# Kernel tuning notes

Measured on AMD Instinct MI355X. Metric: run time of the kernel, lower is better.

Reference implementation:

```python
import jax, jax.numpy as jnp
import numpy as np

INPUT_DIM = 256
UNITS = 256
BATCH = 65536


def _glorot(key, shape):
    fan_in, fan_out = shape
    limit = np.sqrt(6.0 / (fan_in + fan_out)).astype(np.float32)
    return jax.random.uniform(key, shape, jnp.float32, -limit, limit)


def setup_inputs() -> dict:
    key = jax.random.key(0)
    ks = jax.random.split(key, 8)
    d = {
        "inputs": jax.random.normal(ks[0], (BATCH, INPUT_DIM), jnp.float32),
        "h_prev": jax.random.normal(ks[1], (BATCH, UNITS), jnp.float32),
        "c_prev": jax.random.normal(ks[2], (BATCH, UNITS), jnp.float32),
        "W_f": _glorot(ks[3], (INPUT_DIM + UNITS, UNITS)),
        "W_i": _glorot(ks[4], (INPUT_DIM + UNITS, UNITS)),
        "W_c": _glorot(ks[5], (INPUT_DIM + UNITS, UNITS)),
        "W_o": _glorot(ks[6], (INPUT_DIM + UNITS, UNITS)),
        "b_f": jnp.zeros((UNITS,), jnp.float32),
        "b_i": jnp.zeros((UNITS,), jnp.float32),
        "b_c": jnp.zeros((UNITS,), jnp.float32),
        "b_o": jnp.zeros((UNITS,), jnp.float32),
    }
    return d


def reference(inputs, h_prev, c_prev, W_f, W_i, W_c, W_o, b_f, b_i, b_c, b_o):
    # z: [B, input_dim + units]
    z = jnp.concatenate([inputs, h_prev], axis=-1)
    f = jax.nn.sigmoid(z @ W_f + b_f)
    i = jax.nn.sigmoid(z @ W_i + b_i)
    c_tilde = jnp.tanh(z @ W_c + b_c)
    c = f * c_prev + i * c_tilde
    o = jax.nn.sigmoid(z @ W_o + b_o)
    h = o * jnp.tanh(c)
    return h, c
```

## Files before the change

### kernel.cpp

```cpp
#include <hip/hip_runtime.h>
#include <hip/hip_bf16.h>
#include <stdint.h>

#define BATCH   65536
#define UNITS   256
#define NCHUNK  8
#define ROWP    72
#define GSZ     (64 * ROWP)
#define SMEM_BYTES 65536

using f32x16 = __attribute__((ext_vector_type(16))) float;
using bf16x8 = __attribute__((ext_vector_type(8))) short;

__device__ __forceinline__ short f2bf(float f) {
  union { float f; unsigned u; } v; v.f = f;
  unsigned r = v.u + 0x7FFFu + ((v.u >> 16) & 1u);
  return (short)(r >> 16);
}
__device__ __forceinline__ float bf2f(short s) {
  union { float f; unsigned u; } v; v.u = ((unsigned)(unsigned short)s) << 16;
  return v.f;
}
__device__ __forceinline__ unsigned pk2(float a, float b) {
  union { __hip_bfloat162 h; unsigned u; } cv;
  cv.h = __float22bfloat162_rn(make_float2(a, b));
  return cv.u;
}

#define BAR() do { asm volatile("s_waitcnt lgkmcnt(0)" ::: "memory"); \
                   __builtin_amdgcn_s_barrier(); } while (0)

__global__ void cvt_weights(const float* __restrict__ Wf, const float* __restrict__ Wi,
                            const float* __restrict__ Wc, const float* __restrict__ Wo,
                            short* __restrict__ Wt) {
  int idx = blockIdx.x * 256 + threadIdx.x;
  int g   = idx >> 17;
  int k   = (idx >> 8) & 511;
  int col = idx & 255;
  const float* W = (g == 0) ? Wf : (g == 1) ? Wi : (g == 2) ? Wc : Wo;
  float val = W[k * 256 + col];
  int nb = col >> 6, n = col & 63;
  int c = k >> 6, kg = (k >> 3) & 7, k8 = k & 7;
  int out = ((((g * 4 + nb) * 8 + c) * 8 + kg) * 64 + n) * 8 + k8;
  Wt[out] = f2bf(val);
}

__global__ __launch_bounds__(256, 2) void lstm_fused(
    const float* __restrict__ x, const float* __restrict__ hprev,
    const float* __restrict__ cprev, const short* __restrict__ Wt,
    const float* __restrict__ bfp, const float* __restrict__ bip,
    const float* __restrict__ bcp, const float* __restrict__ bop,
    float* __restrict__ hout, float* __restrict__ cout)
{
  extern __shared__ __align__(16) char smem[];
  const int tid  = threadIdx.x;
  const int g    = tid >> 6;
  const int lane = tid & 63;
  const int la   = lane & 31;
  const int hh   = lane >> 5;

  int bid = blockIdx.x;
  int wg  = (bid & 7) * 512 + (bid >> 3);
  const int m0 = (wg >> 2) * 64;
  const int nb = wg & 3;
  const int n0 = nb * 64;

  const short* Bbase = Wt + ((size_t)(g * 4 + nb)) * 32768 + hh * 512 + la * 8;

  f32x16 acc[2][2] = {};
  bf16x8 bregA[8], bregB[8];

  auto loadB = [&](int c, bf16x8* br) {
#pragma unroll
    for (int ks = 0; ks < 4; ++ks) {
      const short* Bc = Bbase + (size_t)c * 4096 + ks * 1024;
      br[2 * ks]     = *(const bf16x8*)(Bc);
      br[2 * ks + 1] = *(const bf16x8*)(Bc + 256);
    }
  };
  auto compute = [&](int c, const bf16x8* br) {
#pragma unroll
    for (int ks = 0; ks < 4; ++ks) {
      const int kg  = c * 8 + 2 * ks + hh;
      const int off = kg * 1024 + ((la * 16) ^ ((kg & 7) << 4));
      bf16x8 a0 = *(const bf16x8*)(smem + off);
      bf16x8 a1 = *(const bf16x8*)(smem + off + 512);
      acc[0][0] = __builtin_amdgcn_mfma_f32_32x32x16_bf16(a0, br[2*ks],   acc[0][0], 0, 0, 0);
      acc[0][1] = __builtin_amdgcn_mfma_f32_32x32x16_bf16(a0, br[2*ks+1], acc[0][1], 0, 0, 0);
      acc[1][0] = __builtin_amdgcn_mfma_f32_32x32x16_bf16(a1, br[2*ks],   acc[1][0], 0, 0, 0);
      acc[1][1] = __builtin_amdgcn_mfma_f32_32x32x16_bf16(a1, br[2*ks+1], acc[1][1], 0, 0, 0);
    }
  };

  loadB(0, bregA);
  {
    const float4* xt = (const float4*)(x     + (size_t)m0 * 256);
    const float4* ht = (const float4*)(hprev + (size_t)m0 * 256);
    float4 vx[16], vh[16];
#pragma unroll
    for (int i = 0; i < 16; ++i) vx[i] = xt[tid + 256 * i];
#pragma unroll
    for (int i = 0; i < 16; ++i) vh[i] = ht[tid + 256 * i];
#pragma unroll
    for (int i = 0; i < 16; ++i) {
      const int idx = tid + 256 * i;
      const int row = idx >> 6, k4 = idx & 63;
      const int kg = k4 >> 1, half = k4 & 1;
      const int sub = (row * 16 + half * 8) ^ ((kg & 7) << 4);
      uint2 ux; ux.x = pk2(vx[i].x, vx[i].y); ux.y = pk2(vx[i].z, vx[i].w);
      *(uint2*)(smem + kg * 1024 + sub) = ux;
      uint2 uh; uh.x = pk2(vh[i].x, vh[i].y); uh.y = pk2(vh[i].z, vh[i].w);
      *(uint2*)(smem + (kg + 32) * 1024 + sub) = uh;
    }
  }
  BAR();

#pragma unroll
  for (int c = 0; c < NCHUNK; ++c) {
    bf16x8* cur = (c & 1) ? bregB : bregA;
    bf16x8* nxt = (c & 1) ? bregA : bregB;
    if (c + 1 < NCHUNK) loadB(c + 1, nxt);
    __builtin_amdgcn_s_setprio(1);
    compute(c, cur);
    __builtin_amdgcn_s_setprio(0);
  }

  const int ccol = tid & 63;
  const int rg   = tid >> 6;
  const size_t gbase = (size_t)(m0 + rg * 16) * 256 + n0 + ccol;
  float cp[16];
#pragma unroll
  for (int j = 0; j < 16; ++j) cp[j] = cprev[gbase + (size_t)j * 256];
  BAR();

  const float* bptr = (g == 0) ? bfp : (g == 1) ? bip : (g == 2) ? bcp : bop;
  const float bias0 = bptr[n0 + la];
  const float bias1 = bptr[n0 + 32 + la];
  short* G = (short*)smem;
#pragma unroll
  for (int mi = 0; mi < 2; ++mi)
#pragma unroll
    for (int ni = 0; ni < 2; ++ni) {
      const float bias = ni ? bias1 : bias0;
      const int   col  = la + ni * 32;
#pragma unroll
      for (int rq = 0; rq < 4; ++rq) {
        const int row0 = rq * 8 + 4 * hh + mi * 32;
        float t[4];
#pragma unroll
        for (int e = 0; e < 4; ++e) {
          float vv = acc[mi][ni][rq * 4 + e] + bias;
          t[e] = (g == 2) ? (1.f - 2.f / (__expf(2.f * vv) + 1.f))
                          : (1.f / (1.f + __expf(-vv)));
        }
        uint2 u; u.x = pk2(t[0], t[1]); u.y = pk2(t[2], t[3]);
        *(uint2*)(G + g * GSZ + col * ROWP + row0) = u;
      }
    }
  BAR();

  {
    const short* Gp = G + ccol * ROWP + rg * 16;
    bf16x8 gf[4][2];
#pragma unroll
    for (int gg = 0; gg < 4; ++gg) {
      gf[gg][0] = *(const bf16x8*)(Gp + gg * GSZ);
      gf[gg][1] = *(const bf16x8*)(Gp + gg * GSZ + 8);
    }
#pragma unroll
    for (int j = 0; j < 16; ++j) {
      float fg = bf2f(gf[0][j >> 3][j & 7]);
      float ig = bf2f(gf[1][j >> 3][j & 7]);
      float cg = bf2f(gf[2][j >> 3][j & 7]);
      float og = bf2f(gf[3][j >> 3][j & 7]);
      float cnew = fg * cp[j] + ig * cg;
      float hnew = og * (1.f - 2.f / (__expf(2.f * cnew) + 1.f));
      hout[gbase + (size_t)j * 256] = hnew;
      cout[gbase + (size_t)j * 256] = cnew;
    }
  }
}

extern "C" void kernel_launch(void* const* d_in, const int* in_sizes, int n_in,
                              void* d_out, int out_size, void* d_ws, size_t ws_size,
                              hipStream_t stream) {
  const float* x     = (const float*)d_in[0];
  const float* hprev = (const float*)d_in[1];
  const float* cprev = (const float*)d_in[2];
  const float* Wf    = (const float*)d_in[3];
  const float* Wi    = (const float*)d_in[4];
  const float* Wc    = (const float*)d_in[5];
  const float* Wo    = (const float*)d_in[6];
  const float* bfp   = (const float*)d_in[7];
  const float* bip   = (const float*)d_in[8];
  const float* bcp   = (const float*)d_in[9];
  const float* bop   = (const float*)d_in[10];
  float* out = (float*)d_out;
  short* Wt  = (short*)d_ws;

  cvt_weights<<<2048, 256, 0, stream>>>(Wf, Wi, Wc, Wo, Wt);

  lstm_fused<<<dim3(4096), dim3(256), SMEM_BYTES, stream>>>(
      x, hprev, cprev, Wt, bfp, bip, bcp, bop,
      out, out + (size_t)BATCH * UNITS);
}
```

Before: 152.9 us.

## Split each gate's column tile across two waves with 4-deep weight prefetch

```diff
diff --git a/kernel.cpp b/kernel.cpp
--- a/kernel.cpp
+++ b/kernel.cpp
@@ -4,7 +4,7 @@
 
 #define BATCH   65536
 #define UNITS   256
-#define NCHUNK  8
+#define NCH     16
 #define ROWP    72
 #define GSZ     (64 * ROWP)
 #define SMEM_BYTES 65536
@@ -26,9 +26,17 @@
   cv.h = __float22bfloat162_rn(make_float2(a, b));
   return cv.u;
 }
+#define LOG2E 1.4426950408889634f
+__device__ __forceinline__ float fast_sigmoid(float x) {
+  return __builtin_amdgcn_rcpf(1.f + __builtin_amdgcn_exp2f(x * -LOG2E));
+}
+__device__ __forceinline__ float fast_tanh(float x) {
+  return 2.f * __builtin_amdgcn_rcpf(1.f + __builtin_amdgcn_exp2f(x * (-2.f * LOG2E))) - 1.f;
+}
 
 #define BAR() do { asm volatile("s_waitcnt lgkmcnt(0)" ::: "memory"); \
                    __builtin_amdgcn_s_barrier(); } while (0)
+#define WAITV(n) asm volatile("s_waitcnt vmcnt(" #n ")" ::: "memory")
 
 __global__ void cvt_weights(const float* __restrict__ Wf, const float* __restrict__ Wi,
                             const float* __restrict__ Wc, const float* __restrict__ Wo,
@@ -39,13 +47,13 @@
   int col = idx & 255;
   const float* W = (g == 0) ? Wf : (g == 1) ? Wi : (g == 2) ? Wc : Wo;
   float val = W[k * 256 + col];
-  int nb = col >> 6, n = col & 63;
-  int c = k >> 6, kg = (k >> 3) & 7, k8 = k & 7;
-  int out = ((((g * 4 + nb) * 8 + c) * 8 + kg) * 64 + n) * 8 + k8;
+  int nt = col >> 5;
+  int c = k >> 5, ks = (k >> 4) & 1, hi = (k >> 3) & 1, e = k & 7;
+  int out = ((((g * 8 + nt) * 16 + c) * 2 + ks) * 64 + hi * 32 + (col & 31)) * 8 + e;
   Wt[out] = f2bf(val);
 }
 
-__global__ __launch_bounds__(256, 2) void lstm_fused(
+__global__ __launch_bounds__(512, 4) void lstm_fused(
     const float* __restrict__ x, const float* __restrict__ hprev,
     const float* __restrict__ cprev, const short* __restrict__ Wt,
     const float* __restrict__ bfp, const float* __restrict__ bip,
@@ -54,7 +62,9 @@
 {
   extern __shared__ __align__(16) char smem[];
   const int tid  = threadIdx.x;
-  const int g    = tid >> 6;
+  const int w    = tid >> 6;
+  const int g    = w & 3;
+  const int nh   = w >> 2;
   const int lane = tid & 63;
   const int la   = lane & 31;
   const int hh   = lane >> 5;
@@ -62,121 +72,105 @@
   int bid = blockIdx.x;
   int wg  = (bid & 7) * 512 + (bid >> 3);
   const int m0 = (wg >> 2) * 64;
-  const int nb = wg & 3;
-  const int n0 = nb * 64;
-
-  const short* Bbase = Wt + ((size_t)(g * 4 + nb)) * 32768 + hh * 512 + la * 8;
-
-  f32x16 acc[2][2] = {};
-  bf16x8 bregA[8], bregB[8];
-
-  auto loadB = [&](int c, bf16x8* br) {
-#pragma unroll
-    for (int ks = 0; ks < 4; ++ks) {
-      const short* Bc = Bbase + (size_t)c * 4096 + ks * 1024;
-      br[2 * ks]     = *(const bf16x8*)(Bc);
-      br[2 * ks + 1] = *(const bf16x8*)(Bc + 256);
+  const int nt = wg & 3;
+  const int n0 = nt * 64;
+
+  const short* Bbase = Wt + (size_t)(g * 8 + nt * 2 + nh) * 16384;
+
+  f32x16 acc[2] = {};
+  bf16x8 bB[4][2];
+
+  auto loadB = [&](int c) {
+    const short* p = Bbase + c * 1024 + lane * 8;
+    bB[c & 3][0] = *(const bf16x8*)(p);
+    bB[c & 3][1] = *(const bf16x8*)(p + 512);
+  };
+
+#pragma unroll
+  for (int i = 0; i < 16; ++i) {
+    const int idx  = tid + 512 * i;
+    const int row  = idx >> 7;
+    const int k4   = idx & 127;
+    const float* src = (k4 < 64)
+        ? (x     + (size_t)(m0 + row) * 256 + k4 * 4)
+        : (hprev + (size_t)(m0 + row) * 256 + (k4 - 64) * 4);
+    float4 v = *(const float4*)src;
+    const int c   = k4 >> 3, ks = (k4 >> 2) & 1, hi2 = (k4 >> 1) & 1;
+    const int e4  = (k4 & 1) * 4;
+    const int mh  = row >> 5, r31 = row & 31;
+    const int swz = (((c << 1) | ks) & 7) << 4;
+    const int byte = ((c * 2 + mh) * 2 + ks) * 1024
+                   + ((hi2 * 512 + r31 * 16) ^ swz) + e4 * 2;
+    uint2 u; u.x = pk2(v.x, v.y); u.y = pk2(v.z, v.w);
+    *(uint2*)(smem + byte) = u;
+  }
+  loadB(0); loadB(1); loadB(2); loadB(3);
+  BAR();
+
+#pragma unroll
+  for (int c = 0; c < NCH; ++c) {
+    if      (c <  NCH - 3) { WAITV(6); }
+    else if (c == NCH - 3) { WAITV(4); }
+    else if (c == NCH - 2) { WAITV(2); }
+    else                   { WAITV(0); }
+#pragma unroll
+    for (int ks = 0; ks < 2; ++ks) {
+      const int swz = (((c << 1) | ks) & 7) << 4;
+      const int b0  = ((c * 2 + 0) * 2 + ks) * 1024 + ((lane * 16) ^ swz);
+      const int b1  = ((c * 2 + 1) * 2 + ks) * 1024 + ((lane * 16) ^ swz);
+      bf16x8 a0 = *(const bf16x8*)(smem + b0);
+      bf16x8 a1 = *(const bf16x8*)(smem + b1);
+      acc[0] = __builtin_amdgcn_mfma_f32_32x32x16_bf16(a0, bB[c & 3][ks], acc[0], 0, 0, 0);
+      acc[1] = __builtin_amdgcn_mfma_f32_32x32x16_bf16(a1, bB[c & 3][ks], acc[1], 0, 0, 0);
     }
-  };
-  auto compute = [&](int c, const bf16x8* br) {
-#pragma unroll
-    for (int ks = 0; ks < 4; ++ks) {
-      const int kg  = c * 8 + 2 * ks + hh;
-      const int off = kg * 1024 + ((la * 16) ^ ((kg & 7) << 4));
-      bf16x8 a0 = *(const bf16x8*)(smem + off);
-      bf16x8 a1 = *(const bf16x8*)(smem + off + 512);
-      acc[0][0] = __builtin_amdgcn_mfma_f32_32x32x16_bf16(a0, br[2*ks],   acc[0][0], 0, 0, 0);
-      acc[0][1] = __builtin_amdgcn_mfma_f32_32x32x16_bf16(a0, br[2*ks+1], acc[0][1], 0, 0, 0);
-      acc[1][0] = __builtin_amdgcn_mfma_f32_32x32x16_bf16(a1, br[2*ks],   acc[1][0], 0, 0, 0);
-      acc[1][1] = __builtin_amdgcn_mfma_f32_32x32x16_bf16(a1, br[2*ks+1], acc[1][1], 0, 0, 0);
+    if (c + 4 < NCH) loadB(c + 4);
+  }
+
+  const int ccol = tid & 63;
+  const int rs   = tid >> 6;
+  const size_t gb = (size_t)(m0 + rs * 8) * 256 + n0 + ccol;
+  BAR();
+
+  float cp[8];
+#pragma unroll
+  for (int j = 0; j < 8; ++j) cp[j] = cprev[gb + (size_t)j * 256];
+
+  const float* bptr = (g == 0) ? bfp : (g == 1) ? bip : (g == 2) ? bcp : bop;
+  const float bias = bptr[n0 + nh * 32 + la];
+  short* G = (short*)smem;
+#pragma unroll
+  for (int mi = 0; mi < 2; ++mi) {
+    const int col = nh * 32 + la;
+#pragma unroll
+    for (int rq = 0; rq < 4; ++rq) {
+      const int row0 = rq * 8 + 4 * hh + mi * 32;
+      float t[4];
+#pragma unroll
+      for (int e = 0; e < 4; ++e) {
+        float vv = acc[mi][rq * 4 + e] + bias;
+        t[e] = (g == 2) ? fast_tanh(vv) : fast_sigmoid(vv);
+      }
+      uint2 u; u.x = pk2(t[0], t[1]); u.y = pk2(t[2], t[3]);
+      *(uint2*)(G + (g * 64 + col) * ROWP + row0) = u;
     }
-  };
-
-  loadB(0, bregA);
+  }
+  BAR();
+
   {
-    const float4* xt = (const float4*)(x     + (size_t)m0 * 256);
-    const float4* ht = (const float4*)(hprev + (size_t)m0 * 256);
-    float4 vx[16], vh[16];
-#pragma unroll
-    for (int i = 0; i < 16; ++i) vx[i] = xt[tid + 256 * i];
-#pragma unroll
-    for (int i = 0; i < 16; ++i) vh[i] = ht[tid + 256 * i];
-#pragma unroll
-    for (int i = 0; i < 16; ++i) {
-      const int idx = tid + 256 * i;
-      const int row = idx >> 6, k4 = idx & 63;
-      const int kg = k4 >> 1, half = k4 & 1;
-      const int sub = (row * 16 + half * 8) ^ ((kg & 7) << 4);
-      uint2 ux; ux.x = pk2(vx[i].x, vx[i].y); ux.y = pk2(vx[i].z, vx[i].w);
-      *(uint2*)(smem + kg * 1024 + sub) = ux;
-      uint2 uh; uh.x = pk2(vh[i].x, vh[i].y); uh.y = pk2(vh[i].z, vh[i].w);
-      *(uint2*)(smem + (kg + 32) * 1024 + sub) = uh;
-    }
-  }
-  BAR();
-
-#pragma unroll
-  for (int c = 0; c < NCHUNK; ++c) {
-    bf16x8* cur = (c & 1) ? bregB : bregA;
-    bf16x8* nxt = (c & 1) ? bregA : bregB;
-    if (c + 1 < NCHUNK) loadB(c + 1, nxt);
-    __builtin_amdgcn_s_setprio(1);
-    compute(c, cur);
-    __builtin_amdgcn_s_setprio(0);
-  }
-
-  const int ccol = tid & 63;
-  const int rg   = tid >> 6;
-  const size_t gbase = (size_t)(m0 + rg * 16) * 256 + n0 + ccol;
-  float cp[16];
-#pragma unroll
-  for (int j = 0; j < 16; ++j) cp[j] = cprev[gbase + (size_t)j * 256];
-  BAR();
-
-  const float* bptr = (g == 0) ? bfp : (g == 1) ? bip : (g == 2) ? bcp : bop;
-  const float bias0 = bptr[n0 + la];
-  const float bias1 = bptr[n0 + 32 + la];
-  short* G = (short*)smem;
-#pragma unroll
-  for (int mi = 0; mi < 2; ++mi)
-#pragma unroll
-    for (int ni = 0; ni < 2; ++ni) {
-      const float bias = ni ? bias1 : bias0;
-      const int   col  = la + ni * 32;
-#pragma unroll
-      for (int rq = 0; rq < 4; ++rq) {
-        const int row0 = rq * 8 + 4 * hh + mi * 32;
-        float t[4];
-#pragma unroll
-        for (int e = 0; e < 4; ++e) {
-          float vv = acc[mi][ni][rq * 4 + e] + bias;
-          t[e] = (g == 2) ? (1.f - 2.f / (__expf(2.f * vv) + 1.f))
-                          : (1.f / (1.f + __expf(-vv)));
-        }
-        uint2 u; u.x = pk2(t[0], t[1]); u.y = pk2(t[2], t[3]);
-        *(uint2*)(G + g * GSZ + col * ROWP + row0) = u;
-      }
-    }
-  BAR();
-
-  {
-    const short* Gp = G + ccol * ROWP + rg * 16;
-    bf16x8 gf[4][2];
-#pragma unroll
-    for (int gg = 0; gg < 4; ++gg) {
-      gf[gg][0] = *(const bf16x8*)(Gp + gg * GSZ);
-      gf[gg][1] = *(const bf16x8*)(Gp + gg * GSZ + 8);
-    }
-#pragma unroll
-    for (int j = 0; j < 16; ++j) {
-      float fg = bf2f(gf[0][j >> 3][j & 7]);
-      float ig = bf2f(gf[1][j >> 3][j & 7]);
-      float cg = bf2f(gf[2][j >> 3][j & 7]);
-      float og = bf2f(gf[3][j >> 3][j & 7]);
+    const short* Gp = G + ccol * ROWP + rs * 8;
+    bf16x8 gf[4];
+#pragma unroll
+    for (int t = 0; t < 4; ++t) gf[t] = *(const bf16x8*)(Gp + t * 64 * ROWP);
+#pragma unroll
+    for (int j = 0; j < 8; ++j) {
+      float fg = bf2f(gf[0][j]);
+      float ig = bf2f(gf[1][j]);
+      float cg = bf2f(gf[2][j]);
+      float og = bf2f(gf[3][j]);
       float cnew = fg * cp[j] + ig * cg;
-      float hnew = og * (1.f - 2.f / (__expf(2.f * cnew) + 1.f));
-      hout[gbase + (size_t)j * 256] = hnew;
-      cout[gbase + (size_t)j * 256] = cnew;
+      float hnew = og * fast_tanh(cnew);
+      hout[gb + (size_t)j * 256] = hnew;
+      cout[gb + (size_t)j * 256] = cnew;
     }
   }
 }
@@ -200,7 +194,7 @@
 
   cvt_weights<<<2048, 256, 0, stream>>>(Wf, Wi, Wc, Wo, Wt);
 
-  lstm_fused<<<dim3(4096), dim3(256), SMEM_BYTES, stream>>>(
+  lstm_fused<<<dim3(4096), dim3(512), SMEM_BYTES, stream>>>(
       x, hprev, cprev, Wt, bfp, bip, bcp, bop,
       out, out + (size_t)BATCH * UNITS);
 }
```

New measurement: 137.1 us. 1.12x faster.
